# Optimization experiments

Hardware: AMD Instinct MI355X
Metric: run time of the kernel (lower is better)

The kernel has to match this reference:

```python
import jax, jax.numpy as jnp
import numpy as np

N_NODES = 50000
N_EDGES = 800000
N_FEAT = 256


def setup_inputs() -> dict:
    key = jax.random.key(0)
    k_h, k_src, k_dst, k_w1, k_w2 = jax.random.split(key, 5)
    h = jax.random.normal(k_h, (N_NODES, N_FEAT), dtype=jnp.float32)
    src = jax.random.randint(k_src, (N_EDGES,), 0, N_NODES, dtype=jnp.int32)
    dst = jax.random.randint(k_dst, (N_EDGES,), 0, N_NODES, dtype=jnp.int32)
    # Kaiming-uniform-ish init like nn.Linear defaults
    b1 = 1.0 / np.sqrt(2 * N_FEAT)
    b2 = 1.0 / np.sqrt(N_FEAT)
    W1_w = jax.random.uniform(k_w1, (N_FEAT, 2 * N_FEAT), dtype=jnp.float32, minval=-b1, maxval=b1)
    W1_b = jnp.zeros((N_FEAT,), dtype=jnp.float32)
    W2_w = jax.random.uniform(k_w2, (1, N_FEAT), dtype=jnp.float32, minval=-b2, maxval=b2)
    W2_b = jnp.zeros((1,), dtype=jnp.float32)
    return {"h": h, "src": src, "dst": dst, "W1_w": W1_w, "W1_b": W1_b, "W2_w": W2_w, "W2_b": W2_b}


def reference(h, src, dst, W1_w, W1_b, W2_w, W2_b):
    # Gather per-edge endpoint features and concat along feature dim: [E, 2F]
    e = jnp.concatenate([h[src], h[dst]], axis=-1)
    # 2-layer MLP: Linear -> ReLU -> Linear, squeeze to per-edge score [E]
    hid = jax.nn.relu(e @ W1_w.T + W1_b)          # [E, F]
    score = (hid @ W2_w.T + W2_b)[:, 0]            # [E]
    return score
```

## Files before the change

### kernel.cpp

```cpp
#include <hip/hip_runtime.h>

#define F 256
#define TWO_F 512
#define BM 128
#define BN 128
#define BK 64

typedef __attribute__((ext_vector_type(8))) short short8;
typedef __attribute__((ext_vector_type(4))) float float4v;

static __device__ __forceinline__ unsigned short f2bf(float f) {
    unsigned u = __float_as_uint(f);
    u += 0x7FFFu + ((u >> 16) & 1u);
    return (unsigned short)(u >> 16);
}
static __device__ __forceinline__ float blo(unsigned u) { return __uint_as_float(u << 16); }
static __device__ __forceinline__ float bhi(unsigned u) { return __uint_as_float(u & 0xFFFF0000u); }

__global__ void prep_w_kernel(const float* __restrict__ W1, unsigned short* __restrict__ Wb) {
    int i = blockIdx.x * blockDim.x + threadIdx.x;
    if (i >= TWO_F * F) return;
    int n = i >> 8;
    int k = i & 255;
    float v = W1[(n & 255) * TWO_F + ((n >> 8) << 8) + k];
    Wb[i] = f2bf(v);
}

__global__ __launch_bounds__(256) void gemm_kernel(
    const float* __restrict__ h, const unsigned short* __restrict__ Wb,
    unsigned short* __restrict__ C, int M)
{
    __shared__ unsigned short sA[BM * BK];
    __shared__ unsigned short sB[BN * BK];

    const int tid  = threadIdx.x;
    const int lane = tid & 63;
    const int wid  = tid >> 6;
    const int wm   = wid >> 1;
    const int wn   = wid & 1;
    const int bm   = blockIdx.x * BM;
    const int bn   = blockIdx.y * BN;

    const int ar = tid >> 1;
    const int ak = (tid & 1) * 32;
    const bool a_ok = (bm + ar) < M;
    const float* hrow = h + (size_t)(bm + ar) * F + ak;

    const int brow0 = wid * 32;
    const int b_r   = lane >> 3;
    const int b_k   = (lane & 7) * 8;

    float4v acc[4][4];
    #pragma unroll
    for (int i = 0; i < 4; ++i)
        #pragma unroll
        for (int j = 0; j < 4; ++j)
            acc[i][j] = (float4v)(0.f);

    const int quad = lane >> 4;
    const int l15  = lane & 15;

    for (int k0 = 0; k0 < F; k0 += BK) {
        #pragma unroll
        for (int p = 0; p < 4; ++p) {
            int r = brow0 + p * 8;
            const unsigned short* gp = Wb + (size_t)(bn + r + b_r) * F + k0 + b_k;
            __builtin_amdgcn_global_load_lds(
                (const __attribute__((address_space(1))) unsigned int*)gp,
                (__attribute__((address_space(3))) unsigned int*)&sB[r * BK],
                16, 0, 0);
        }

        float4 av[8];
        if (a_ok) {
            const float* p = hrow + k0;
            #pragma unroll
            for (int i = 0; i < 8; ++i) av[i] = *(const float4*)(p + i * 4);
        } else {
            #pragma unroll
            for (int i = 0; i < 8; ++i) av[i] = make_float4(0.f, 0.f, 0.f, 0.f);
        }
        #pragma unroll
        for (int i2 = 0; i2 < 4; ++i2) {
            union { unsigned short us[8]; uint4 v; } pk;
            pk.us[0] = f2bf(av[2 * i2].x);
            pk.us[1] = f2bf(av[2 * i2].y);
            pk.us[2] = f2bf(av[2 * i2].z);
            pk.us[3] = f2bf(av[2 * i2].w);
            pk.us[4] = f2bf(av[2 * i2 + 1].x);
            pk.us[5] = f2bf(av[2 * i2 + 1].y);
            pk.us[6] = f2bf(av[2 * i2 + 1].z);
            pk.us[7] = f2bf(av[2 * i2 + 1].w);
            *(uint4*)&sA[ar * BK + ak + i2 * 8] = pk.v;
        }
        __syncthreads();

        #pragma unroll
        for (int ks = 0; ks < 2; ++ks) {
            short8 afr[4], bfr[4];
            #pragma unroll
            for (int mt = 0; mt < 4; ++mt)
                afr[mt] = *(const short8*)&sA[(wm * 64 + mt * 16 + l15) * BK + ks * 32 + quad * 8];
            #pragma unroll
            for (int nt = 0; nt < 4; ++nt)
                bfr[nt] = *(const short8*)&sB[(wn * 64 + nt * 16 + l15) * BK + ks * 32 + quad * 8];
            #pragma unroll
            for (int mt = 0; mt < 4; ++mt)
                #pragma unroll
                for (int nt = 0; nt < 4; ++nt)
                    acc[mt][nt] = __builtin_amdgcn_mfma_f32_16x16x32_bf16(
                        afr[mt], bfr[nt], acc[mt][nt], 0, 0, 0);
        }
        __syncthreads();
    }

    #pragma unroll
    for (int mt = 0; mt < 4; ++mt) {
        int gm0 = bm + wm * 64 + mt * 16 + quad * 4;
        #pragma unroll
        for (int r = 0; r < 4; ++r) {
            int gm = gm0 + r;
            if (gm < M) {
                unsigned short* cp = C + (size_t)gm * TWO_F + bn + wn * 64 + l15;
                #pragma unroll
                for (int nt = 0; nt < 4; ++nt)
                    cp[nt * 16] = f2bf(acc[mt][nt][r]);
            }
        }
    }
}

__global__ __launch_bounds__(256) void edge_kernel(
    const unsigned short* __restrict__ C,
    const int* __restrict__ src, const int* __restrict__ dst,
    const float* __restrict__ w2, const float* __restrict__ b1v,
    const float* __restrict__ b2, float* __restrict__ out, int E)
{
    const int lane = threadIdx.x & 31;
    const int e = blockIdx.x * 8 + (threadIdx.x >> 5);
    if (e >= E) return;
    const int s = src[e];
    const int d = dst[e];

    uint4 av = *(const uint4*)(C + (size_t)s * TWO_F + lane * 8);
    uint4 bv = *(const uint4*)(C + (size_t)d * TWO_F + F + lane * 8);
    float4 w0 = *(const float4*)(w2 + lane * 8);
    float4 w1 = *(const float4*)(w2 + lane * 8 + 4);
    float4 c0 = *(const float4*)(b1v + lane * 8);
    float4 c1 = *(const float4*)(b1v + lane * 8 + 4);

    float sum;
    sum  = w0.x * fmaxf(blo(av.x) + blo(bv.x) + c0.x, 0.f);
    sum += w0.y * fmaxf(bhi(av.x) + bhi(bv.x) + c0.y, 0.f);
    sum += w0.z * fmaxf(blo(av.y) + blo(bv.y) + c0.z, 0.f);
    sum += w0.w * fmaxf(bhi(av.y) + bhi(bv.y) + c0.w, 0.f);
    sum += w1.x * fmaxf(blo(av.z) + blo(bv.z) + c1.x, 0.f);
    sum += w1.y * fmaxf(bhi(av.z) + bhi(bv.z) + c1.y, 0.f);
    sum += w1.z * fmaxf(blo(av.w) + blo(bv.w) + c1.z, 0.f);
    sum += w1.w * fmaxf(bhi(av.w) + bhi(bv.w) + c1.w, 0.f);

    #pragma unroll
    for (int off = 16; off > 0; off >>= 1)
        sum += __shfl_down(sum, off, 32);

    if (lane == 0) out[e] = sum + b2[0];
}

extern "C" void kernel_launch(void* const* d_in, const int* in_sizes, int n_in,
                              void* d_out, int out_size, void* d_ws, size_t ws_size,
                              hipStream_t stream) {
    const float* h    = (const float*)d_in[0];
    const int*   src  = (const int*)d_in[1];
    const int*   dst  = (const int*)d_in[2];
    const float* W1_w = (const float*)d_in[3];
    const float* W1_b = (const float*)d_in[4];
    const float* W2_w = (const float*)d_in[5];
    const float* W2_b = (const float*)d_in[6];
    float* out = (float*)d_out;

    const int M = in_sizes[0] / F;
    const int E = in_sizes[1];

    unsigned short* Wb = (unsigned short*)d_ws;
    unsigned short* C  = (unsigned short*)((char*)d_ws + 512 * 1024);

    prep_w_kernel<<<(TWO_F * F + 255) / 256, 256, 0, stream>>>(W1_w, Wb);

    dim3 ggrid((M + BM - 1) / BM, TWO_F / BN);
    gemm_kernel<<<ggrid, 256, 0, stream>>>(h, Wb, C, M);

    edge_kernel<<<(E + 7) / 8, 256, 0, stream>>>(C, src, dst, W2_w, W1_b, W2_b, out, E);
}
```

Baseline: 244.5 us.

## Widen GEMM N tile, pad LDS A, fold bias into GEMM output

The GEMM N tile grows from 128 to 256 so each block converts and loads the A rows of h half as often, and the grid halves along N. The A tile in LDS gets a padded row stride to cut bank conflicts, and the fp32-to-bf16 packing now uses a cheaper round-and-perm sequence. The out-of-range row branch becomes a clamp. The layer-1 bias is added in the GEMM epilogue, the edge kernel drops its bias loads, and it reads high halves raw without masking, which adds a little low-bit noise. The larger accumulator array (128 floats per thread) raises register pressure and may lower occupancy.

```diff
diff --git a/kernel.cpp b/kernel.cpp
--- a/kernel.cpp
+++ b/kernel.cpp
@@ -3,8 +3,9 @@
 #define F 256
 #define TWO_F 512
 #define BM 128
-#define BN 128
+#define BN 256
 #define BK 64
+#define ASTR 72
 
 typedef __attribute__((ext_vector_type(8))) short short8;
 typedef __attribute__((ext_vector_type(4))) float float4v;
@@ -14,8 +15,13 @@
     u += 0x7FFFu + ((u >> 16) & 1u);
     return (unsigned short)(u >> 16);
 }
+static __device__ __forceinline__ unsigned pack2(float lo, float hi) {
+    unsigned a = __float_as_uint(lo) + 0x8000u;
+    unsigned b = __float_as_uint(hi) + 0x8000u;
+    return __builtin_amdgcn_perm(b, a, 0x07060302u);
+}
 static __device__ __forceinline__ float blo(unsigned u) { return __uint_as_float(u << 16); }
-static __device__ __forceinline__ float bhi(unsigned u) { return __uint_as_float(u & 0xFFFF0000u); }
+static __device__ __forceinline__ float rawf(unsigned u) { return __uint_as_float(u); }
 
 __global__ void prep_w_kernel(const float* __restrict__ W1, unsigned short* __restrict__ Wb) {
     int i = blockIdx.x * blockDim.x + threadIdx.x;
@@ -28,9 +34,9 @@
 
 __global__ __launch_bounds__(256) void gemm_kernel(
     const float* __restrict__ h, const unsigned short* __restrict__ Wb,
-    unsigned short* __restrict__ C, int M)
+    const float* __restrict__ b1v, unsigned short* __restrict__ C, int M)
 {
-    __shared__ unsigned short sA[BM * BK];
+    __shared__ unsigned short sA[BM * ASTR];
     __shared__ unsigned short sB[BN * BK];
 
     const int tid  = threadIdx.x;
@@ -43,26 +49,25 @@
 
     const int ar = tid >> 1;
     const int ak = (tid & 1) * 32;
-    const bool a_ok = (bm + ar) < M;
-    const float* hrow = h + (size_t)(bm + ar) * F + ak;
+    int arow = bm + ar; if (arow > M - 1) arow = M - 1;
+    const float* hrow = h + (size_t)arow * F + ak;
 
-    const int brow0 = wid * 32;
+    const int brow0 = wid * 64;
     const int b_r   = lane >> 3;
     const int b_k   = (lane & 7) * 8;
 
-    float4v acc[4][4];
+    float4v acc[4][8];
     #pragma unroll
     for (int i = 0; i < 4; ++i)
         #pragma unroll
-        for (int j = 0; j < 4; ++j)
-            acc[i][j] = (float4v)(0.f);
+        for (int j = 0; j < 8; ++j) acc[i][j] = (float4v)(0.f);
 
     const int quad = lane >> 4;
     const int l15  = lane & 15;
 
     for (int k0 = 0; k0 < F; k0 += BK) {
         #pragma unroll
-        for (int p = 0; p < 4; ++p) {
+        for (int p = 0; p < 8; ++p) {
             int r = brow0 + p * 8;
             const unsigned short* gp = Wb + (size_t)(bn + r + b_r) * F + k0 + b_k;
             __builtin_amdgcn_global_load_lds(
@@ -71,49 +76,48 @@
                 16, 0, 0);
         }
 
-        float4 av[8];
-        if (a_ok) {
-            const float* p = hrow + k0;
-            #pragma unroll
-            for (int i = 0; i < 8; ++i) av[i] = *(const float4*)(p + i * 4);
-        } else {
-            #pragma unroll
-            for (int i = 0; i < 8; ++i) av[i] = make_float4(0.f, 0.f, 0.f, 0.f);
-        }
+        const float* p = hrow + k0;
         #pragma unroll
-        for (int i2 = 0; i2 < 4; ++i2) {
-            union { unsigned short us[8]; uint4 v; } pk;
-            pk.us[0] = f2bf(av[2 * i2].x);
-            pk.us[1] = f2bf(av[2 * i2].y);
-            pk.us[2] = f2bf(av[2 * i2].z);
-            pk.us[3] = f2bf(av[2 * i2].w);
-            pk.us[4] = f2bf(av[2 * i2 + 1].x);
-            pk.us[5] = f2bf(av[2 * i2 + 1].y);
-            pk.us[6] = f2bf(av[2 * i2 + 1].z);
-            pk.us[7] = f2bf(av[2 * i2 + 1].w);
-            *(uint4*)&sA[ar * BK + ak + i2 * 8] = pk.v;
+        for (int half = 0; half < 2; ++half) {
+            float4 a0 = *(const float4*)(p + half * 16 + 0);
+            float4 a1 = *(const float4*)(p + half * 16 + 4);
+            float4 a2 = *(const float4*)(p + half * 16 + 8);
+            float4 a3 = *(const float4*)(p + half * 16 + 12);
+            uint4 q0, q1;
+            q0.x = pack2(a0.x, a0.y); q0.y = pack2(a0.z, a0.w);
+            q0.z = pack2(a1.x, a1.y); q0.w = pack2(a1.z, a1.w);
+            q1.x = pack2(a2.x, a2.y); q1.y = pack2(a2.z, a2.w);
+            q1.z = pack2(a3.x, a3.y); q1.w = pack2(a3.z, a3.w);
+            *(uint4*)&sA[ar * ASTR + ak + half * 16 + 0] = q0;
+            *(uint4*)&sA[ar * ASTR + ak + half * 16 + 8] = q1;
         }
         __syncthreads();
 
         #pragma unroll
         for (int ks = 0; ks < 2; ++ks) {
-            short8 afr[4], bfr[4];
+            short8 afr[4], bfr[8];
             #pragma unroll
             for (int mt = 0; mt < 4; ++mt)
-                afr[mt] = *(const short8*)&sA[(wm * 64 + mt * 16 + l15) * BK + ks * 32 + quad * 8];
+                afr[mt] = *(const short8*)&sA[(wm * 64 + mt * 16 + l15) * ASTR + ks * 32 + quad * 8];
             #pragma unroll
-            for (int nt = 0; nt < 4; ++nt)
-                bfr[nt] = *(const short8*)&sB[(wn * 64 + nt * 16 + l15) * BK + ks * 32 + quad * 8];
+            for (int nt = 0; nt < 8; ++nt)
+                bfr[nt] = *(const short8*)&sB[(wn * 128 + nt * 16 + l15) * BK + ks * 32 + quad * 8];
             #pragma unroll
             for (int mt = 0; mt < 4; ++mt)
                 #pragma unroll
-                for (int nt = 0; nt < 4; ++nt)
+                for (int nt = 0; nt < 8; ++nt)
                     acc[mt][nt] = __builtin_amdgcn_mfma_f32_16x16x32_bf16(
                         afr[mt], bfr[nt], acc[mt][nt], 0, 0, 0);
         }
         __syncthreads();
     }
 
+    float bias[8];
+    #pragma unroll
+    for (int nt = 0; nt < 8; ++nt) {
+        int n = bn + wn * 128 + nt * 16 + l15;
+        bias[nt] = (n < F) ? b1v[n] : 0.f;
+    }
     #pragma unroll
     for (int mt = 0; mt < 4; ++mt) {
         int gm0 = bm + wm * 64 + mt * 16 + quad * 4;
@@ -121,10 +125,10 @@
         for (int r = 0; r < 4; ++r) {
             int gm = gm0 + r;
             if (gm < M) {
-                unsigned short* cp = C + (size_t)gm * TWO_F + bn + wn * 64 + l15;
+                unsigned short* cp = C + (size_t)gm * TWO_F + bn + wn * 128 + l15;
                 #pragma unroll
-                for (int nt = 0; nt < 4; ++nt)
-                    cp[nt * 16] = f2bf(acc[mt][nt][r]);
+                for (int nt = 0; nt < 8; ++nt)
+                    cp[nt * 16] = f2bf(acc[mt][nt][r] + bias[nt]);
             }
         }
     }
@@ -133,7 +137,7 @@
 __global__ __launch_bounds__(256) void edge_kernel(
     const unsigned short* __restrict__ C,
     const int* __restrict__ src, const int* __restrict__ dst,
-    const float* __restrict__ w2, const float* __restrict__ b1v,
+    const float* __restrict__ w2,
     const float* __restrict__ b2, float* __restrict__ out, int E)
 {
     const int lane = threadIdx.x & 31;
@@ -146,18 +150,16 @@
     uint4 bv = *(const uint4*)(C + (size_t)d * TWO_F + F + lane * 8);
     float4 w0 = *(const float4*)(w2 + lane * 8);
     float4 w1 = *(const float4*)(w2 + lane * 8 + 4);
-    float4 c0 = *(const float4*)(b1v + lane * 8);
-    float4 c1 = *(const float4*)(b1v + lane * 8 + 4);
 
     float sum;
-    sum  = w0.x * fmaxf(blo(av.x) + blo(bv.x) + c0.x, 0.f);
-    sum += w0.y * fmaxf(bhi(av.x) + bhi(bv.x) + c0.y, 0.f);
-    sum += w0.z * fmaxf(blo(av.y) + blo(bv.y) + c0.z, 0.f);
-    sum += w0.w * fmaxf(bhi(av.y) + bhi(bv.y) + c0.w, 0.f);
-    sum += w1.x * fmaxf(blo(av.z) + blo(bv.z) + c1.x, 0.f);
-    sum += w1.y * fmaxf(bhi(av.z) + bhi(bv.z) + c1.y, 0.f);
-    sum += w1.z * fmaxf(blo(av.w) + blo(bv.w) + c1.z, 0.f);
-    sum += w1.w * fmaxf(bhi(av.w) + bhi(bv.w) + c1.w, 0.f);
+    sum  = w0.x * fmaxf(blo(av.x) + blo(bv.x), 0.f);
+    sum += w0.y * fmaxf(rawf(av.x) + rawf(bv.x), 0.f);
+    sum += w0.z * fmaxf(blo(av.y) + blo(bv.y), 0.f);
+    sum += w0.w * fmaxf(rawf(av.y) + rawf(bv.y), 0.f);
+    sum += w1.x * fmaxf(blo(av.z) + blo(bv.z), 0.f);
+    sum += w1.y * fmaxf(rawf(av.z) + rawf(bv.z), 0.f);
+    sum += w1.z * fmaxf(blo(av.w) + blo(bv.w), 0.f);
+    sum += w1.w * fmaxf(rawf(av.w) + rawf(bv.w), 0.f);
 
     #pragma unroll
     for (int off = 16; off > 0; off >>= 1)
@@ -187,7 +189,7 @@
     prep_w_kernel<<<(TWO_F * F + 255) / 256, 256, 0, stream>>>(W1_w, Wb);
 
     dim3 ggrid((M + BM - 1) / BM, TWO_F / BN);
-    gemm_kernel<<<ggrid, 256, 0, stream>>>(h, Wb, C, M);
+    gemm_kernel<<<ggrid, 256, 0, stream>>>(h, Wb, W1_b, C, M);
 
-    edge_kernel<<<(E + 7) / 8, 256, 0, stream>>>(C, src, dst, W2_w, W1_b, W2_b, out, E);
+    edge_kernel<<<(E + 7) / 8, 256, 0, stream>>>(C, src, dst, W2_w, W2_b, out, E);
 }
```

After: 259.0 us. 1.06x slower.
